# Optimization experiments

Measured on AMD Instinct MI355X. Metric: run time of the kernel, lower is better.

Reference implementation:

```python
import jax, jax.numpy as jnp
import numpy as np

DIM = 1024
HEADS = 16
HEAD_DIM = DIM // HEADS
EPS = 1e-5


def setup_inputs() -> dict:
    key = jax.random.key(0)
    ks = jax.random.split(key, 4)
    N, L = 4, 2048
    x = jax.random.normal(ks[0], (N, L, DIM), dtype=jnp.float32)
    # causal mask: True means masked (strictly upper triangle)
    attn_mask = jnp.triu(jnp.ones((L, L), dtype=jnp.bool_), k=1)[None, None, :, :]
    w_qkv = jax.random.normal(ks[1], (3 * DIM, DIM), dtype=jnp.float32) * (DIM ** -0.5)
    w_proj = jax.random.normal(ks[2], (DIM, DIM), dtype=jnp.float32) * (DIM ** -0.5)
    b_proj = jnp.zeros((DIM,), dtype=jnp.float32)
    q_gamma = jnp.ones((HEAD_DIM,), dtype=jnp.float32)
    q_beta = jnp.zeros((HEAD_DIM,), dtype=jnp.float32)
    k_gamma = jnp.ones((HEAD_DIM,), dtype=jnp.float32)
    k_beta = jnp.zeros((HEAD_DIM,), dtype=jnp.float32)
    return {"x": x, "attn_mask": attn_mask, "w_qkv": w_qkv, "w_proj": w_proj,
            "b_proj": b_proj, "q_gamma": q_gamma, "q_beta": q_beta,
            "k_gamma": k_gamma, "k_beta": k_beta}


def _layernorm(h, gamma, beta):
    mu = jnp.mean(h, axis=-1, keepdims=True)
    var = jnp.mean(jnp.square(h - mu), axis=-1, keepdims=True)
    return (h - mu) * jax.lax.rsqrt(var + EPS) * gamma + beta


def reference(x, attn_mask, w_qkv, w_proj, b_proj, q_gamma, q_beta, k_gamma, k_beta):
    N, L, D = x.shape
    H, hd = HEADS, HEAD_DIM
    scale = hd ** -0.5
    qkv = jnp.einsum('nld,ed->nle', x, w_qkv)  # [N, L, 3D]
    qkv = qkv.reshape(N, L, 3, H, hd).transpose(2, 0, 3, 1, 4)  # [3, N, H, L, hd]
    q, k, v = qkv[0], qkv[1], qkv[2]
    q = _layernorm(q, q_gamma, q_beta)
    k = _layernorm(k, k_gamma, k_beta)
    scores = jnp.einsum('nhqd,nhkd->nhqk', q * scale, k)
    scores = scores + jnp.where(attn_mask, -jnp.inf, 0.0).astype(scores.dtype)
    attn = jax.nn.softmax(scores, axis=-1)
    out = jnp.einsum('nhqk,nhkd->nhqd', attn, v)  # [N, H, L, hd]
    out = out.transpose(0, 2, 1, 3).reshape(N, L, D)
    return jnp.einsum('nld,ed->nle', out, w_proj) + b_proj
```

## Files before the change

kernel.cpp:

```cpp
#include <hip/hip_runtime.h>


using f16x8 = __attribute__((ext_vector_type(8))) _Float16;
using f16x4 = __attribute__((ext_vector_type(4))) _Float16;
using f16x2 = __attribute__((ext_vector_type(2))) _Float16;
using f32x4 = __attribute__((ext_vector_type(4))) float;
using f32x16 = __attribute__((ext_vector_type(16))) float;
using u32x4 = __attribute__((ext_vector_type(4))) unsigned int;

#define MFMA16(a, b, c) __builtin_amdgcn_mfma_f32_16x16x32_f16(a, b, c, 0, 0, 0)
#define MFMA32(a, b, c) __builtin_amdgcn_mfma_f32_32x32x16_f16(a, b, c, 0, 0, 0)

__device__ __forceinline__ void gload_lds16(const void* g, void* l) {
  __builtin_amdgcn_global_load_lds(
      (const __attribute__((address_space(1))) unsigned int*)g,
      (__attribute__((address_space(3))) unsigned int*)l, 16, 0, 0);
}

__device__ __forceinline__ float dot2acc(unsigned int pk, float c) {
#if __has_builtin(__builtin_amdgcn_fdot2)
  const f16x2 ones = {(_Float16)1.f, (_Float16)1.f};
  return __builtin_amdgcn_fdot2(__builtin_bit_cast(f16x2, pk), ones, c, false);
#else
  f16x2 v = __builtin_bit_cast(f16x2, pk);
  return c + (float)v[0] + (float)v[1];
#endif
}

__global__ __launch_bounds__(256) void convert_all_kernel(
    const float* __restrict__ x, const float* __restrict__ wq,
    const float* __restrict__ wp, _Float16* __restrict__ xb,
    _Float16* __restrict__ wqb, _Float16* __restrict__ wpb) {
  long i = ((long)blockIdx.x * 256 + threadIdx.x) * 8;
  const float* src;
  _Float16* dst;
  if (i < 8388608) {
    src = x; dst = xb;
  } else if (i < 8388608 + 3145728) {
    src = wq + (i - 8388608); dst = wqb + (i - 8388608); i = 0;
  } else {
    src = wp + (i - 11534336); dst = wpb + (i - 11534336); i = 0;
  }
  float4 a = *(const float4*)(src + i);
  float4 b = *(const float4*)(src + i + 4);
  f16x8 o;
  o[0] = (_Float16)a.x; o[1] = (_Float16)a.y; o[2] = (_Float16)a.z; o[3] = (_Float16)a.w;
  o[4] = (_Float16)b.x; o[5] = (_Float16)b.y; o[6] = (_Float16)b.z; o[7] = (_Float16)b.w;
  *(f16x8*)(dst + i) = o;
}

template <int MODE>
__global__ __launch_bounds__(256, 3) void gemm_bt(
    const _Float16* __restrict__ A, const _Float16* __restrict__ B,
    void* __restrict__ Cout, _Float16* __restrict__ Vt,
    const float* __restrict__ bias,
    const float* __restrict__ qg, const float* __restrict__ qb,
    const float* __restrict__ kg, const float* __restrict__ kb,
    int M, int N, int K) {
  __shared__ __align__(16) char smem[49152];
  const int tid = threadIdx.x;
  const int w = tid >> 6, lane = tid & 63;
  const int c = lane & 15, g = lane >> 4;
  const long mbase = (long)blockIdx.x * 128;
  const int by = (MODE == 1) ? (int)((blockIdx.y + 16) % 24) : (int)blockIdx.y;
  const long nbase = (long)by * 128;
  const int wm = (w >> 1) * 64, wn = (w & 1) * 64;
  const int sr4 = lane >> 2;
  const int scol = ((lane & 3) ^ ((lane >> 3) & 3)) * 8;
  const int sg = (g ^ ((c >> 1) & 3)) * 8;
  const char* pAr = smem + (wm + c) * 64 + sg * 2;
  const char* pBr = smem + 24576 + (wn + c) * 64 + sg * 2;

#define GSTAGE(off_, kt_)                                                     \
  {                                                                           \
    const int kk_ = (kt_) * 32;                                               \
    _Pragma("unroll") for (int i = 0; i < 2; ++i) {                           \
      const int arow = w * 32 + i * 16 + sr4;                                 \
      gload_lds16(A + (mbase + arow) * K + kk_ + scol,                        \
                  smem + (off_) + (w * 2 + i) * 1024);                        \
    }                                                                         \
    _Pragma("unroll") for (int j = 0; j < 2; ++j) {                           \
      const int brow = w * 32 + j * 16 + sr4;                                 \
      gload_lds16(B + (nbase + brow) * K + kk_ + scol,                        \
                  smem + 24576 + (off_) + (w * 2 + j) * 1024);                \
    }                                                                         \
  }

  f32x4 acc[4][4];
#pragma unroll
  for (int i = 0; i < 4; ++i)
#pragma unroll
    for (int j = 0; j < 4; ++j) acc[i][j] = f32x4{0.f, 0.f, 0.f, 0.f};

  const int nk = K >> 5;
  GSTAGE(0, 0);
  GSTAGE(8192, 1);
  int rOff = 0, sOff = 16384;
  for (int kt = 0; kt < nk; ++kt) {
    if (kt + 1 < nk) {
      asm volatile("s_waitcnt vmcnt(4)" ::: "memory");
    } else {
      asm volatile("s_waitcnt vmcnt(0)" ::: "memory");
    }
    __builtin_amdgcn_sched_barrier(0);
    __builtin_amdgcn_s_barrier();
    __builtin_amdgcn_sched_barrier(0);
    f16x8 af[4], bfr[4];
#pragma unroll
    for (int mt = 0; mt < 4; ++mt)
      af[mt] = *(const f16x8*)(pAr + rOff + mt * 1024);
#pragma unroll
    for (int nt = 0; nt < 4; ++nt)
      bfr[nt] = *(const f16x8*)(pBr + rOff + nt * 1024);
    if (kt + 2 < nk) GSTAGE(sOff, kt + 2);
#pragma unroll
    for (int mt = 0; mt < 4; ++mt)
#pragma unroll
      for (int nt = 0; nt < 4; ++nt)
        acc[mt][nt] = MFMA16(af[mt], bfr[nt], acc[mt][nt]);
    rOff = (rOff == 16384) ? 0 : rOff + 8192;
    sOff = (sOff == 16384) ? 0 : sOff + 8192;
  }
#undef GSTAGE

  if constexpr (MODE == 1) {
    const int region = by >> 3;
    if (region == 2) {
      __syncthreads();
      _Float16* T = (_Float16*)smem;
#pragma unroll
      for (int nt = 0; nt < 4; ++nt) {
        const int dloc = wn + nt * 16 + c;
#pragma unroll
        for (int mt = 0; mt < 4; ++mt) {
          const int lloc = wm + mt * 16 + g * 4;
          f16x4 o;
#pragma unroll
          for (int r = 0; r < 4; ++r) o[r] = (_Float16)acc[mt][nt][r];
          *(f16x4*)(T + dloc * 136 + lloc) = o;
        }
      }
      __syncthreads();
      const long n = mbase >> 11;
      const long lbase = mbase & 2047;
      const int chunk = tid & 15;
      const int rbase = tid >> 4;
#pragma unroll
      for (int i = 0; i < 8; ++i) {
        const int row = rbase + i * 16;
        const long dcol = (nbase - 2048) + row;
        *(f16x8*)(Vt + (n * 1024 + dcol) * 2048 + lbase + chunk * 8) =
            *(const f16x8*)(T + row * 136 + chunk * 8);
      }
      return;
    }
    const float* gamma = region ? kg : qg;
    const float* beta = region ? kb : qb;
    float gam[4], bet[4];
#pragma unroll
    for (int nt = 0; nt < 4; ++nt) {
      gam[nt] = gamma[nt * 16 + c];
      bet[nt] = beta[nt * 16 + c];
    }
    const float sc = region ? 1.f : 0.1803368801111204f;
#pragma unroll
    for (int mt = 0; mt < 4; ++mt)
#pragma unroll
      for (int r = 0; r < 4; ++r) {
        float s1 = 0.f, s2 = 0.f;
#pragma unroll
        for (int nt = 0; nt < 4; ++nt) {
          const float v = acc[mt][nt][r];
          s1 += v;
          s2 += v * v;
        }
#pragma unroll
        for (int msk = 1; msk < 16; msk <<= 1) {
          s1 += __shfl_xor(s1, msk);
          s2 += __shfl_xor(s2, msk);
        }
        const float mu = s1 * 0.015625f;
        const float rstd = rsqrtf(s2 * 0.015625f - mu * mu + 1e-5f);
#pragma unroll
        for (int nt = 0; nt < 4; ++nt)
          acc[mt][nt][r] =
              ((acc[mt][nt][r] - mu) * rstd * gam[nt] + bet[nt]) * sc;
      }
#pragma unroll
    for (int nt = 0; nt < 4; ++nt) {
      const long col = nbase + wn + nt * 16 + c;
#pragma unroll
      for (int mt = 0; mt < 4; ++mt)
#pragma unroll
        for (int r = 0; r < 4; ++r) {
          const long row = mbase + wm + mt * 16 + g * 4 + r;
          ((_Float16*)Cout)[row * N + col] = (_Float16)acc[mt][nt][r];
        }
    }
  } else {
#pragma unroll
    for (int nt = 0; nt < 4; ++nt) {
      const long col = nbase + wn + nt * 16 + c;
      const float bv = bias ? bias[col] : 0.f;
#pragma unroll
      for (int mt = 0; mt < 4; ++mt)
#pragma unroll
        for (int r = 0; r < 4; ++r) {
          const long row = mbase + wm + mt * 16 + g * 4 + r;
          ((float*)Cout)[row * N + col] = acc[mt][nt][r] + bv;
        }
    }
  }
}

__global__ __launch_bounds__(256, 3) void attn_kernel(
    const _Float16* __restrict__ qkv, const _Float16* __restrict__ Vt,
    _Float16* __restrict__ Ob) {
  __shared__ __align__(16) char lds[49152];
  const int w = threadIdx.x >> 6;
  const int lane = threadIdx.x & 63;
  const int c5 = lane & 31;
  const int hi = lane >> 5;
  const int lin = (int)(blockIdx.x + 64 * blockIdx.y);
  const int nh = (lin & 7) * 8 + ((lin >> 3) & 7);
  const long n = nh >> 4;
  const int h = nh & 15;
  const int qtile = 15 - (lin >> 6);
  const int qlo_blk = qtile * 128;
  const int qlo = qlo_blk + w * 32;
  const int qrow = qlo + c5;

  const _Float16* Qp = qkv + n * 2048 * 3072 + h * 64;
  const _Float16* Kq = Qp + 1024;
  const _Float16* Vp = Vt + (long)nh * 64 * 2048;

  const int sr8 = lane >> 3;
  const int scol = ((lane & 7) ^ sr8) * 8;

  const int nkv_blk = (qlo_blk + 191) >> 6;
  const int nkv_w = (qlo + 95) >> 6;

#define STAGE(OFF, kv_)                                                        \
  {                                                                            \
    const int kb_ = (kv_) * 64;                                                \
    _Pragma("unroll") for (int i = 0; i < 2; ++i) {                            \
      const int idx = w * 2 + i;                                               \
      const int row = idx * 8 + sr8;                                           \
      gload_lds16(Kq + (long)(kb_ + row) * 3072 + scol,                        \
                  lds + (OFF) + idx * 1024);                                   \
      gload_lds16(Vp + (long)row * 2048 + kb_ + scol,                          \
                  lds + (OFF) + 8192 + idx * 1024);                            \
    }                                                                          \
  }

  f16x8 qf[4];
#pragma unroll
  for (int dc = 0; dc < 4; ++dc)
    qf[dc] = *(const f16x8*)(Qp + (long)qrow * 3072 + dc * 16 + hi * 8);

  f32x16 negM;
#pragma unroll
  for (int r = 0; r < 16; ++r) negM[r] = -12.0f;

  f32x16 acc[2];
#pragma unroll
  for (int db = 0; db < 2; ++db)
#pragma unroll
    for (int r = 0; r < 16; ++r) acc[db][r] = 0.f;
  float ls = 0.f;

  const int swr = c5 & 7;
  const char* Lb[4];
#pragma unroll
  for (int j = 0; j < 4; ++j)
    Lb[j] = lds + c5 * 128 + (((j * 2 + hi) ^ swr) << 4);

#define COMPUTE(OFF, kv_)                                                      \
  {                                                                            \
    const int kbase = (kv_) * 64;                                              \
    f32x16 s0, s1;                                                             \
    __builtin_amdgcn_s_setprio(1);                                             \
    {                                                                          \
      f16x8 kf0 = *(const f16x8*)(Lb[0] + (OFF));                              \
      f16x8 kf1 = *(const f16x8*)(Lb[0] + (OFF) + 4096);                       \
      s0 = MFMA32(kf0, qf[0], negM);                                           \
      s1 = MFMA32(kf1, qf[0], negM);                                           \
    }                                                                          \
    _Pragma("unroll") for (int dc = 1; dc < 4; ++dc) {                         \
      f16x8 kf0 = *(const f16x8*)(Lb[dc] + (OFF));                             \
      f16x8 kf1 = *(const f16x8*)(Lb[dc] + (OFF) + 4096);                      \
      s0 = MFMA32(kf0, qf[dc], s0);                                            \
      s1 = MFMA32(kf1, qf[dc], s1);                                            \
    }                                                                          \
    __builtin_amdgcn_s_setprio(0);                                             \
    if (kbase + 63 > qlo) {                                                    \
      _Pragma("unroll") for (int r = 0; r < 16; ++r) {                         \
        const int mv = (r & 3) + 8 * (r >> 2) + 4 * hi;                        \
        if (kbase + mv > qrow) s0[r] = -1e30f;                                 \
        if (kbase + 32 + mv > qrow) s1[r] = -1e30f;                            \
      }                                                                        \
    }                                                                          \
    _Pragma("unroll") for (int r = 0; r < 16; ++r) {                           \
      s0[r] = exp2f(s0[r]);                                                    \
      s1[r] = exp2f(s1[r]);                                                    \
    }                                                                          \
    unsigned int pk0[4][2], pk1[4][2];                                         \
    _Pragma("unroll") for (int r2 = 0; r2 < 4; ++r2)                           \
        _Pragma("unroll") for (int p = 0; p < 2; ++p) {                        \
      pk0[r2][p] = __builtin_bit_cast(                                         \
          unsigned int, __builtin_amdgcn_cvt_pkrtz(s0[4 * r2 + 2 * p],         \
                                                   s0[4 * r2 + 2 * p + 1]));   \
      pk1[r2][p] = __builtin_bit_cast(                                         \
          unsigned int, __builtin_amdgcn_cvt_pkrtz(s1[4 * r2 + 2 * p],         \
                                                   s1[4 * r2 + 2 * p + 1]));   \
    }                                                                          \
    _Pragma("unroll") for (int r2 = 0; r2 < 4; ++r2)                           \
        _Pragma("unroll") for (int p = 0; p < 2; ++p) {                        \
      ls = dot2acc(pk0[r2][p], ls);                                            \
      ls = dot2acc(pk1[r2][p], ls);                                            \
    }                                                                          \
    f16x8 pB[4];                                                               \
    _Pragma("unroll") for (int kk = 0; kk < 4; ++kk) {                         \
      const int rx = (kk & 1) * 2;                                             \
      unsigned int x0 = (kk < 2) ? pk0[rx][0] : pk1[rx][0];                    \
      unsigned int y0 = (kk < 2) ? pk0[rx + 1][0] : pk1[rx + 1][0];            \
      unsigned int x1 = (kk < 2) ? pk0[rx][1] : pk1[rx][1];                    \
      unsigned int y1 = (kk < 2) ? pk0[rx + 1][1] : pk1[rx + 1][1];            \
      asm("v_permlane32_swap_b32 %0, %1" : "+v"(x0), "+v"(y0));                \
      asm("v_permlane32_swap_b32 %0, %1" : "+v"(x1), "+v"(y1));                \
      pB[kk] = __builtin_bit_cast(f16x8, u32x4{x0, x1, y0, y1});               \
    }                                                                          \
    __builtin_amdgcn_s_setprio(1);                                             \
    _Pragma("unroll") for (int db = 0; db < 2; ++db)                           \
        _Pragma("unroll") for (int kk = 0; kk < 4; ++kk) {                     \
      f16x8 vf = *(const f16x8*)(Lb[kk] + (OFF) + 8192 + db * 4096);           \
      acc[db] = MFMA32(vf, pB[kk], acc[db]);                                   \
    }                                                                          \
    __builtin_amdgcn_s_setprio(0);                                             \
  }

  STAGE(0, 0);
  STAGE(16384, 1);
  int rOff = 0, sOff = 32768;
  for (int kv = 0; kv < nkv_blk; ++kv) {
    if (kv + 1 < nkv_blk) {
      asm volatile("s_waitcnt vmcnt(4)" ::: "memory");
    } else {
      asm volatile("s_waitcnt vmcnt(0)" ::: "memory");
    }
    __builtin_amdgcn_sched_barrier(0);
    __builtin_amdgcn_s_barrier();
    __builtin_amdgcn_sched_barrier(0);
    if (kv + 2 < nkv_blk) STAGE(sOff, kv + 2);
    if (kv < nkv_w) COMPUTE(rOff, kv);
    rOff = (rOff == 32768) ? 0 : rOff + 16384;
    sOff = (sOff == 32768) ? 0 : sOff + 16384;
  }
#undef COMPUTE
#undef STAGE

  const float lsr = ls + __shfl_xor(ls, 32);
  const float inv = 1.f / lsr;
  _Float16* ob = Ob + ((long)(n * 2048) + qrow) * 1024 + h * 64 + 4 * hi;
#pragma unroll
  for (int db = 0; db < 2; ++db)
#pragma unroll
    for (int r2 = 0; r2 < 4; ++r2) {
      f16x4 o;
#pragma unroll
      for (int j = 0; j < 4; ++j)
        o[j] = (_Float16)(acc[db][4 * r2 + j] * inv);
      *(f16x4*)(ob + db * 32 + 8 * r2) = o;
    }
}

extern "C" void kernel_launch(void* const* d_in, const int* in_sizes, int n_in,
                              void* d_out, int out_size, void* d_ws, size_t ws_size,
                              hipStream_t stream) {
  const float* x = (const float*)d_in[0];
  const float* w_qkv = (const float*)d_in[2];
  const float* w_proj = (const float*)d_in[3];
  const float* b_proj = (const float*)d_in[4];
  const float* qg = (const float*)d_in[5];
  const float* qb = (const float*)d_in[6];
  const float* kg = (const float*)d_in[7];
  const float* kb = (const float*)d_in[8];

  char* ws = (char*)d_ws;
  _Float16* xb     = (_Float16*)(ws + 0);
  _Float16* wqkvb  = (_Float16*)(ws + 16777216);
  _Float16* wprojb = (_Float16*)(ws + 23068672);
  _Float16* qkvh   = (_Float16*)(ws + 25165824);
  _Float16* Vt     = (_Float16*)(ws + 75497472);
  _Float16* Ob     = xb;

  convert_all_kernel<<<6144, 256, 0, stream>>>(x, w_qkv, w_proj,
                                               xb, wqkvb, wprojb);

  gemm_bt<1><<<dim3(64, 24), 256, 0, stream>>>(xb, wqkvb, qkvh, Vt, nullptr,
                                               qg, qb, kg, kb, 8192, 3072, 1024);
  attn_kernel<<<dim3(64, 16), 256, 0, stream>>>(qkvh, Vt, Ob);
  gemm_bt<0><<<dim3(64, 8), 256, 0, stream>>>(Ob, wprojb, d_out, nullptr, b_proj,
                                              nullptr, nullptr, nullptr, nullptr,
                                              8192, 1024, 1024);
}
```

Measured before the change: 186.3 us.

## Give each wave its own LDS pipeline and 32-key tiles, removing block barriers

Each wave now stages its own K/V tiles into a private 16KB LDS region with double buffering over 32-key tiles. Block-wide barriers go away and each wave iterates only up to its own causal limit, instead of sharing 64-key tiles across the block. The costs are that the four waves load K/V redundantly instead of sharing, LDS rises to 64KB, and the launch bound drops to 2 blocks per CU. MFMA work per tile is halved, so loop overhead and wait points double.

```diff
diff --git a/kernel.cpp b/kernel.cpp
--- a/kernel.cpp
+++ b/kernel.cpp
@@ -213,10 +213,10 @@
   }
 }
 
-__global__ __launch_bounds__(256, 3) void attn_kernel(
+__global__ __launch_bounds__(256, 2) void attn_kernel(
     const _Float16* __restrict__ qkv, const _Float16* __restrict__ Vt,
     _Float16* __restrict__ Ob) {
-  __shared__ __align__(16) char lds[49152];
+  __shared__ __align__(16) char lds[65536];
   const int w = threadIdx.x >> 6;
   const int lane = threadIdx.x & 63;
   const int c5 = lane & 31;
@@ -226,30 +226,31 @@
   const long n = nh >> 4;
   const int h = nh & 15;
   const int qtile = 15 - (lin >> 6);
-  const int qlo_blk = qtile * 128;
-  const int qlo = qlo_blk + w * 32;
+  const int unit = qtile * 4 + w;
+  const int qlo = unit * 32;
   const int qrow = qlo + c5;
 
   const _Float16* Qp = qkv + n * 2048 * 3072 + h * 64;
   const _Float16* Kq = Qp + 1024;
   const _Float16* Vp = Vt + (long)nh * 64 * 2048;
 
+  char* myLds = lds + w * 16384;
   const int sr8 = lane >> 3;
   const int scol = ((lane & 7) ^ sr8) * 8;
-
-  const int nkv_blk = (qlo_blk + 191) >> 6;
-  const int nkv_w = (qlo + 95) >> 6;
-
-#define STAGE(OFF, kv_)                                                        \
+  const int vscol = ((lane & 3) ^ ((lane >> 3) & 3)) * 8;
+
+  const int nkv = unit + 1;
+
+#define STAGE(BOFF, t_)                                                        \
   {                                                                            \
-    const int kb_ = (kv_) * 64;                                                \
-    _Pragma("unroll") for (int i = 0; i < 2; ++i) {                            \
-      const int idx = w * 2 + i;                                               \
-      const int row = idx * 8 + sr8;                                           \
-      gload_lds16(Kq + (long)(kb_ + row) * 3072 + scol,                        \
-                  lds + (OFF) + idx * 1024);                                   \
-      gload_lds16(Vp + (long)row * 2048 + kb_ + scol,                          \
-                  lds + (OFF) + 8192 + idx * 1024);                            \
+    const int kb_ = (t_) * 32;                                                 \
+    _Pragma("unroll") for (int i = 0; i < 4; ++i) {                            \
+      const int krow = i * 8 + sr8;                                            \
+      gload_lds16(Kq + (long)(kb_ + krow) * 3072 + scol,                       \
+                  myLds + (BOFF) + i * 1024);                                  \
+      const int vrow = i * 16 + (lane >> 2);                                   \
+      gload_lds16(Vp + (long)vrow * 2048 + kb_ + vscol,                        \
+                  myLds + (BOFF) + 4096 + i * 1024);                           \
     }                                                                          \
   }
 
@@ -270,91 +271,83 @@
   float ls = 0.f;
 
   const int swr = c5 & 7;
-  const char* Lb[4];
+  const int vxor = (c5 >> 1) & 3;
+  const char* Lk[4];
 #pragma unroll
   for (int j = 0; j < 4; ++j)
-    Lb[j] = lds + c5 * 128 + (((j * 2 + hi) ^ swr) << 4);
-
-#define COMPUTE(OFF, kv_)                                                      \
+    Lk[j] = myLds + c5 * 128 + (((j * 2 + hi) ^ swr) << 4);
+  const char* Lv[4];
+#pragma unroll
+  for (int db = 0; db < 2; ++db)
+#pragma unroll
+    for (int kk = 0; kk < 2; ++kk)
+      Lv[db * 2 + kk] = myLds + 4096 + (db * 32 + c5) * 64 +
+                        (((kk * 2 + hi) ^ vxor) << 4);
+
+#define COMPUTE(BOFF, t_)                                                      \
   {                                                                            \
-    const int kbase = (kv_) * 64;                                              \
-    f32x16 s0, s1;                                                             \
+    const int kbase = (t_) * 32;                                               \
+    f32x16 s0;                                                                 \
     __builtin_amdgcn_s_setprio(1);                                             \
     {                                                                          \
-      f16x8 kf0 = *(const f16x8*)(Lb[0] + (OFF));                              \
-      f16x8 kf1 = *(const f16x8*)(Lb[0] + (OFF) + 4096);                       \
-      s0 = MFMA32(kf0, qf[0], negM);                                           \
-      s1 = MFMA32(kf1, qf[0], negM);                                           \
+      f16x8 kf = *(const f16x8*)(Lk[0] + (BOFF));                              \
+      s0 = MFMA32(kf, qf[0], negM);                                            \
     }                                                                          \
     _Pragma("unroll") for (int dc = 1; dc < 4; ++dc) {                         \
-      f16x8 kf0 = *(const f16x8*)(Lb[dc] + (OFF));                             \
-      f16x8 kf1 = *(const f16x8*)(Lb[dc] + (OFF) + 4096);                      \
-      s0 = MFMA32(kf0, qf[dc], s0);                                            \
-      s1 = MFMA32(kf1, qf[dc], s1);                                            \
+      f16x8 kf = *(const f16x8*)(Lk[dc] + (BOFF));                             \
+      s0 = MFMA32(kf, qf[dc], s0);                                             \
     }                                                                          \
     __builtin_amdgcn_s_setprio(0);                                             \
-    if (kbase + 63 > qlo) {                                                    \
+    if (kbase + 31 > qlo) {                                                    \
       _Pragma("unroll") for (int r = 0; r < 16; ++r) {                         \
         const int mv = (r & 3) + 8 * (r >> 2) + 4 * hi;                        \
         if (kbase + mv > qrow) s0[r] = -1e30f;                                 \
-        if (kbase + 32 + mv > qrow) s1[r] = -1e30f;                            \
       }                                                                        \
     }                                                                          \
-    _Pragma("unroll") for (int r = 0; r < 16; ++r) {                           \
-      s0[r] = exp2f(s0[r]);                                                    \
-      s1[r] = exp2f(s1[r]);                                                    \
-    }                                                                          \
-    unsigned int pk0[4][2], pk1[4][2];                                         \
+    _Pragma("unroll") for (int r = 0; r < 16; ++r) s0[r] = exp2f(s0[r]);       \
+    unsigned int pk0[4][2];                                                    \
     _Pragma("unroll") for (int r2 = 0; r2 < 4; ++r2)                           \
         _Pragma("unroll") for (int p = 0; p < 2; ++p) {                        \
       pk0[r2][p] = __builtin_bit_cast(                                         \
           unsigned int, __builtin_amdgcn_cvt_pkrtz(s0[4 * r2 + 2 * p],         \
                                                    s0[4 * r2 + 2 * p + 1]));   \
-      pk1[r2][p] = __builtin_bit_cast(                                         \
-          unsigned int, __builtin_amdgcn_cvt_pkrtz(s1[4 * r2 + 2 * p],         \
-                                                   s1[4 * r2 + 2 * p + 1]));   \
-    }                                                                          \
-    _Pragma("unroll") for (int r2 = 0; r2 < 4; ++r2)                           \
-        _Pragma("unroll") for (int p = 0; p < 2; ++p) {                        \
       ls = dot2acc(pk0[r2][p], ls);                                            \
-      ls = dot2acc(pk1[r2][p], ls);                                            \
-    }                                                                          \
-    f16x8 pB[4];                                                               \
-    _Pragma("unroll") for (int kk = 0; kk < 4; ++kk) {                         \
-      const int rx = (kk & 1) * 2;                                             \
-      unsigned int x0 = (kk < 2) ? pk0[rx][0] : pk1[rx][0];                    \
-      unsigned int y0 = (kk < 2) ? pk0[rx + 1][0] : pk1[rx + 1][0];            \
-      unsigned int x1 = (kk < 2) ? pk0[rx][1] : pk1[rx][1];                    \
-      unsigned int y1 = (kk < 2) ? pk0[rx + 1][1] : pk1[rx + 1][1];            \
+    }                                                                          \
+    f16x8 pB[2];                                                               \
+    _Pragma("unroll") for (int kk = 0; kk < 2; ++kk) {                         \
+      const int rx = kk * 2;                                                   \
+      unsigned int x0 = pk0[rx][0];                                            \
+      unsigned int y0 = pk0[rx + 1][0];                                        \
+      unsigned int x1 = pk0[rx][1];                                            \
+      unsigned int y1 = pk0[rx + 1][1];                                        \
       asm("v_permlane32_swap_b32 %0, %1" : "+v"(x0), "+v"(y0));                \
       asm("v_permlane32_swap_b32 %0, %1" : "+v"(x1), "+v"(y1));                \
       pB[kk] = __builtin_bit_cast(f16x8, u32x4{x0, x1, y0, y1});               \
     }                                                                          \
     __builtin_amdgcn_s_setprio(1);                                             \
     _Pragma("unroll") for (int db = 0; db < 2; ++db)                           \
-        _Pragma("unroll") for (int kk = 0; kk < 4; ++kk) {                     \
-      f16x8 vf = *(const f16x8*)(Lb[kk] + (OFF) + 8192 + db * 4096);           \
+        _Pragma("unroll") for (int kk = 0; kk < 2; ++kk) {                     \
+      f16x8 vf = *(const f16x8*)(Lv[db * 2 + kk] + (BOFF));                    \
       acc[db] = MFMA32(vf, pB[kk], acc[db]);                                   \
     }                                                                          \
     __builtin_amdgcn_s_setprio(0);                                             \
   }
 
   STAGE(0, 0);
-  STAGE(16384, 1);
-  int rOff = 0, sOff = 32768;
-  for (int kv = 0; kv < nkv_blk; ++kv) {
-    if (kv + 1 < nkv_blk) {
-      asm volatile("s_waitcnt vmcnt(4)" ::: "memory");
+  if (nkv > 1) STAGE(8192, 1);
+  for (int t = 0; t < nkv; ++t) {
+    if (t + 1 < nkv) {
+      asm volatile("s_waitcnt vmcnt(8)" ::: "memory");
     } else {
       asm volatile("s_waitcnt vmcnt(0)" ::: "memory");
     }
     __builtin_amdgcn_sched_barrier(0);
-    __builtin_amdgcn_s_barrier();
-    __builtin_amdgcn_sched_barrier(0);
-    if (kv + 2 < nkv_blk) STAGE(sOff, kv + 2);
-    if (kv < nkv_w) COMPUTE(rOff, kv);
-    rOff = (rOff == 32768) ? 0 : rOff + 16384;
-    sOff = (sOff == 32768) ? 0 : sOff + 16384;
+    COMPUTE((t & 1) * 8192, t);
+    if (t + 2 < nkv) {
+      asm volatile("s_waitcnt lgkmcnt(0)" ::: "memory");
+      __builtin_amdgcn_sched_barrier(0);
+      STAGE((t & 1) * 8192, t + 2);
+    }
   }
 #undef COMPUTE
 #undef STAGE
```

Measured after the change: 203.4 us. 9.2% more time.

## Rewrite QKV GEMM with 256x256 tiles, 512 threads and phased LDS pipeline

Applied to the files above, without the earlier changes.

Replaces the templated 128x128 GEMM for the QKV projection with a dedicated kernel that uses 256x256 output tiles, 8 waves and 128 KB of LDS double-buffering over 64-wide K steps. The loads for the next K step are split into four phases, interleaved with MFMA work, and gated by explicit vmcnt waits, barriers and s_setprio. The aim is more data reuse per loaded byte and better overlap of global-to-LDS copies with matrix math. The cost is a grid of only 384 blocks, which may hurt occupancy and wave balance. The V-transpose epilogue is reworked to run in two passes, and the output projection becomes a separate non-templated kernel.

```diff
diff --git a/kernel.cpp b/kernel.cpp
--- a/kernel.cpp
+++ b/kernel.cpp
@@ -49,21 +49,205 @@
   *(f16x8*)(dst + i) = o;
 }
 
-template <int MODE>
-__global__ __launch_bounds__(256, 3) void gemm_bt(
+__global__ __launch_bounds__(512, 2) void gemm_qkv(
     const _Float16* __restrict__ A, const _Float16* __restrict__ B,
-    void* __restrict__ Cout, _Float16* __restrict__ Vt,
-    const float* __restrict__ bias,
+    _Float16* __restrict__ qkvh, _Float16* __restrict__ Vt,
     const float* __restrict__ qg, const float* __restrict__ qb,
-    const float* __restrict__ kg, const float* __restrict__ kb,
+    const float* __restrict__ kg, const float* __restrict__ kb) {
+  __shared__ __align__(16) char smem[131072];
+  const int tid = threadIdx.x;
+  const int w = tid >> 6, lane = tid & 63;
+  const int c = lane & 15, g = lane >> 4;
+  const int wr = w >> 2, wc = w & 3;
+  const long mbase = (long)blockIdx.x * 256;
+  const int by = (int)((blockIdx.y + 8) % 12);
+  const long nbase = (long)by * 256;
+  const int srow = tid >> 3;
+  const int scol = ((tid & 7) ^ ((tid >> 3) & 7)) * 8;
+  const int swr8 = c & 7;
+  const char* LA[2];
+  const char* LB[2];
+#pragma unroll
+  for (int ks = 0; ks < 2; ++ks) {
+    LA[ks] = smem + wr * 16384 + c * 128 + (((ks * 4 + g) ^ swr8) << 4);
+    LB[ks] = smem + 65536 + (wc >> 1) * 16384 + ((wc & 1) * 64 + c) * 128 +
+             (((ks * 4 + g) ^ swr8) << 4);
+  }
+
+#define ST_A(DD, HH, RR, KT)                                                  \
+  gload_lds16(                                                                \
+      A + (mbase + (HH) * 128 + (RR) * 64 + srow) * 1024 + (KT) * 64 + scol,  \
+      smem + (DD) + (HH) * 16384 + (RR) * 8192 + w * 1024)
+#define ST_B(DD, HH, RR, KT)                                                  \
+  gload_lds16(                                                                \
+      B + (nbase + (HH) * 128 + (RR) * 64 + srow) * 1024 + (KT) * 64 + scol,  \
+      smem + 65536 + (DD) + (HH) * 16384 + (RR) * 8192 + w * 1024)
+
+  f32x4 acc[8][4];
+#pragma unroll
+  for (int i = 0; i < 8; ++i)
+#pragma unroll
+    for (int j = 0; j < 4; ++j) acc[i][j] = f32x4{0.f, 0.f, 0.f, 0.f};
+
+#define PHASE(P)                                                              \
+  {                                                                           \
+    f16x8 bf0[4], bf1[4], af00, af01, af10, af11;                             \
+    _Pragma("unroll") for (int nt = 0; nt < 4; ++nt) {                        \
+      bf0[nt] = *(const f16x8*)(LB[0] + rd + nt * 2048);                      \
+      bf1[nt] = *(const f16x8*)(LB[1] + rd + nt * 2048);                      \
+    }                                                                         \
+    af00 = *(const f16x8*)(LA[0] + rd + (2 * (P)) * 2048);                    \
+    af01 = *(const f16x8*)(LA[1] + rd + (2 * (P)) * 2048);                    \
+    af10 = *(const f16x8*)(LA[0] + rd + (2 * (P) + 1) * 2048);                \
+    af11 = *(const f16x8*)(LA[1] + rd + (2 * (P) + 1) * 2048);                \
+    __builtin_amdgcn_s_setprio(1);                                            \
+    _Pragma("unroll") for (int nt = 0; nt < 4; ++nt) {                        \
+      acc[2 * (P)][nt] = MFMA16(af00, bf0[nt], acc[2 * (P)][nt]);             \
+      acc[2 * (P)][nt] = MFMA16(af01, bf1[nt], acc[2 * (P)][nt]);             \
+      acc[2 * (P) + 1][nt] = MFMA16(af10, bf0[nt], acc[2 * (P) + 1][nt]);     \
+      acc[2 * (P) + 1][nt] = MFMA16(af11, bf1[nt], acc[2 * (P) + 1][nt]);     \
+    }                                                                         \
+    __builtin_amdgcn_s_setprio(0);                                            \
+  }
+
+#define BARRIER()                      \
+  __builtin_amdgcn_sched_barrier(0);   \
+  __builtin_amdgcn_s_barrier();        \
+  __builtin_amdgcn_sched_barrier(0)
+
+  const int nk = 16;
+  ST_B(0, 0, 0, 0); ST_B(0, 0, 1, 0); ST_B(0, 1, 0, 0); ST_B(0, 1, 1, 0);
+  ST_A(0, 0, 0, 0); ST_A(0, 1, 0, 0); ST_A(0, 0, 1, 0); ST_A(0, 1, 1, 0);
+  int rd = 0, sd = 32768;
+  for (int kt = 0; kt < nk; ++kt) {
+    const bool more = (kt + 1 < nk);
+    asm volatile("s_waitcnt vmcnt(2)" ::: "memory");
+    BARRIER();
+    if (more) { ST_B(sd, 0, 0, kt + 1); ST_B(sd, 0, 1, kt + 1); }
+    PHASE(0);
+    if (more) {
+      asm volatile("s_waitcnt vmcnt(4)" ::: "memory");
+    } else {
+      asm volatile("s_waitcnt vmcnt(2)" ::: "memory");
+    }
+    BARRIER();
+    if (more) { ST_B(sd, 1, 0, kt + 1); ST_B(sd, 1, 1, kt + 1); }
+    PHASE(1);
+    if (more) {
+      asm volatile("s_waitcnt vmcnt(4)" ::: "memory");
+    } else {
+      asm volatile("s_waitcnt vmcnt(0)" ::: "memory");
+    }
+    BARRIER();
+    if (more) { ST_A(sd, 0, 0, kt + 1); ST_A(sd, 1, 0, kt + 1); }
+    PHASE(2);
+    if (more) {
+      asm volatile("s_waitcnt vmcnt(6)" ::: "memory");
+    } else {
+      asm volatile("s_waitcnt vmcnt(0)" ::: "memory");
+    }
+    BARRIER();
+    if (more) { ST_A(sd, 0, 1, kt + 1); ST_A(sd, 1, 1, kt + 1); }
+    PHASE(3);
+    rd ^= 32768;
+    sd ^= 32768;
+  }
+#undef PHASE
+#undef BARRIER
+#undef ST_A
+#undef ST_B
+
+  const int region = by >> 2;
+  if (region == 2) {
+    __syncthreads();
+    _Float16* T = (_Float16*)smem;
+    const long n = mbase >> 11;
+    const long lbase = mbase & 2047;
+    const int chunk = tid & 31;
+    const int rbase = tid >> 5;
+#pragma unroll
+    for (int p2 = 0; p2 < 2; ++p2) {
+      if ((wc >> 1) == p2) {
+#pragma unroll
+        for (int nt = 0; nt < 4; ++nt) {
+          const int dloc = (wc & 1) * 64 + nt * 16 + c;
+#pragma unroll
+          for (int mt = 0; mt < 8; ++mt) {
+            const int lloc = wr * 128 + mt * 16 + g * 4;
+            f16x4 o;
+#pragma unroll
+            for (int r = 0; r < 4; ++r) o[r] = (_Float16)acc[mt][nt][r];
+            *(f16x4*)(T + dloc * 264 + lloc) = o;
+          }
+        }
+      }
+      __syncthreads();
+#pragma unroll
+      for (int i = 0; i < 8; ++i) {
+        const int row = rbase + i * 16;
+        const long dcol = (nbase - 2048) + p2 * 128 + row;
+        *(f16x8*)(Vt + (n * 1024 + dcol) * 2048 + lbase + chunk * 8) =
+            *(const f16x8*)(T + row * 264 + chunk * 8);
+      }
+      __syncthreads();
+    }
+    return;
+  }
+  const float* gamma = region ? kg : qg;
+  const float* beta = region ? kb : qb;
+  float gam[4], bet[4];
+#pragma unroll
+  for (int nt = 0; nt < 4; ++nt) {
+    gam[nt] = gamma[nt * 16 + c];
+    bet[nt] = beta[nt * 16 + c];
+  }
+  const float sc = region ? 1.f : 0.1803368801111204f;
+#pragma unroll
+  for (int mt = 0; mt < 8; ++mt)
+#pragma unroll
+    for (int r = 0; r < 4; ++r) {
+      float s1 = 0.f, s2 = 0.f;
+#pragma unroll
+      for (int nt = 0; nt < 4; ++nt) {
+        const float v = acc[mt][nt][r];
+        s1 += v;
+        s2 += v * v;
+      }
+#pragma unroll
+      for (int msk = 1; msk < 16; msk <<= 1) {
+        s1 += __shfl_xor(s1, msk);
+        s2 += __shfl_xor(s2, msk);
+      }
+      const float mu = s1 * 0.015625f;
+      const float rstd = rsqrtf(s2 * 0.015625f - mu * mu + 1e-5f);
+#pragma unroll
+      for (int nt = 0; nt < 4; ++nt)
+        acc[mt][nt][r] =
+            ((acc[mt][nt][r] - mu) * rstd * gam[nt] + bet[nt]) * sc;
+    }
+#pragma unroll
+  for (int nt = 0; nt < 4; ++nt) {
+    const long col = nbase + wc * 64 + nt * 16 + c;
+#pragma unroll
+    for (int mt = 0; mt < 8; ++mt)
+#pragma unroll
+      for (int r = 0; r < 4; ++r) {
+        const long row = mbase + wr * 128 + mt * 16 + g * 4 + r;
+        qkvh[row * 3072 + col] = (_Float16)acc[mt][nt][r];
+      }
+  }
+}
+
+__global__ __launch_bounds__(256, 3) void gemm_proj(
+    const _Float16* __restrict__ A, const _Float16* __restrict__ B,
+    float* __restrict__ Cout, const float* __restrict__ bias,
     int M, int N, int K) {
   __shared__ __align__(16) char smem[49152];
   const int tid = threadIdx.x;
   const int w = tid >> 6, lane = tid & 63;
   const int c = lane & 15, g = lane >> 4;
   const long mbase = (long)blockIdx.x * 128;
-  const int by = (MODE == 1) ? (int)((blockIdx.y + 16) % 24) : (int)blockIdx.y;
-  const long nbase = (long)by * 128;
+  const long nbase = (long)blockIdx.y * 128;
   const int wm = (w >> 1) * 64, wn = (w & 1) * 64;
   const int sr4 = lane >> 2;
   const int scol = ((lane & 3) ^ ((lane >> 3) & 3)) * 8;
@@ -123,93 +307,17 @@
   }
 #undef GSTAGE
 
-  if constexpr (MODE == 1) {
-    const int region = by >> 3;
-    if (region == 2) {
-      __syncthreads();
-      _Float16* T = (_Float16*)smem;
-#pragma unroll
-      for (int nt = 0; nt < 4; ++nt) {
-        const int dloc = wn + nt * 16 + c;
-#pragma unroll
-        for (int mt = 0; mt < 4; ++mt) {
-          const int lloc = wm + mt * 16 + g * 4;
-          f16x4 o;
-#pragma unroll
-          for (int r = 0; r < 4; ++r) o[r] = (_Float16)acc[mt][nt][r];
-          *(f16x4*)(T + dloc * 136 + lloc) = o;
-        }
+#pragma unroll
+  for (int nt = 0; nt < 4; ++nt) {
+    const long col = nbase + wn + nt * 16 + c;
+    const float bv = bias ? bias[col] : 0.f;
+#pragma unroll
+    for (int mt = 0; mt < 4; ++mt)
+#pragma unroll
+      for (int r = 0; r < 4; ++r) {
+        const long row = mbase + wm + mt * 16 + g * 4 + r;
+        Cout[row * N + col] = acc[mt][nt][r] + bv;
       }
-      __syncthreads();
-      const long n = mbase >> 11;
-      const long lbase = mbase & 2047;
-      const int chunk = tid & 15;
-      const int rbase = tid >> 4;
-#pragma unroll
-      for (int i = 0; i < 8; ++i) {
-        const int row = rbase + i * 16;
-        const long dcol = (nbase - 2048) + row;
-        *(f16x8*)(Vt + (n * 1024 + dcol) * 2048 + lbase + chunk * 8) =
-            *(const f16x8*)(T + row * 136 + chunk * 8);
-      }
-      return;
-    }
-    const float* gamma = region ? kg : qg;
-    const float* beta = region ? kb : qb;
-    float gam[4], bet[4];
-#pragma unroll
-    for (int nt = 0; nt < 4; ++nt) {
-      gam[nt] = gamma[nt * 16 + c];
-      bet[nt] = beta[nt * 16 + c];
-    }
-    const float sc = region ? 1.f : 0.1803368801111204f;
-#pragma unroll
-    for (int mt = 0; mt < 4; ++mt)
-#pragma unroll
-      for (int r = 0; r < 4; ++r) {
-        float s1 = 0.f, s2 = 0.f;
-#pragma unroll
-        for (int nt = 0; nt < 4; ++nt) {
-          const float v = acc[mt][nt][r];
-          s1 += v;
-          s2 += v * v;
-        }
-#pragma unroll
-        for (int msk = 1; msk < 16; msk <<= 1) {
-          s1 += __shfl_xor(s1, msk);
-          s2 += __shfl_xor(s2, msk);
-        }
-        const float mu = s1 * 0.015625f;
-        const float rstd = rsqrtf(s2 * 0.015625f - mu * mu + 1e-5f);
-#pragma unroll
-        for (int nt = 0; nt < 4; ++nt)
-          acc[mt][nt][r] =
-              ((acc[mt][nt][r] - mu) * rstd * gam[nt] + bet[nt]) * sc;
-      }
-#pragma unroll
-    for (int nt = 0; nt < 4; ++nt) {
-      const long col = nbase + wn + nt * 16 + c;
-#pragma unroll
-      for (int mt = 0; mt < 4; ++mt)
-#pragma unroll
-        for (int r = 0; r < 4; ++r) {
-          const long row = mbase + wm + mt * 16 + g * 4 + r;
-          ((_Float16*)Cout)[row * N + col] = (_Float16)acc[mt][nt][r];
-        }
-    }
-  } else {
-#pragma unroll
-    for (int nt = 0; nt < 4; ++nt) {
-      const long col = nbase + wn + nt * 16 + c;
-      const float bv = bias ? bias[col] : 0.f;
-#pragma unroll
-      for (int mt = 0; mt < 4; ++mt)
-#pragma unroll
-        for (int r = 0; r < 4; ++r) {
-          const long row = mbase + wm + mt * 16 + g * 4 + r;
-          ((float*)Cout)[row * N + col] = acc[mt][nt][r] + bv;
-        }
-    }
   }
 }
 
@@ -397,10 +505,9 @@
   convert_all_kernel<<<6144, 256, 0, stream>>>(x, w_qkv, w_proj,
                                                xb, wqkvb, wprojb);
 
-  gemm_bt<1><<<dim3(64, 24), 256, 0, stream>>>(xb, wqkvb, qkvh, Vt, nullptr,
-                                               qg, qb, kg, kb, 8192, 3072, 1024);
+  gemm_qkv<<<dim3(32, 12), 512, 0, stream>>>(xb, wqkvb, qkvh, Vt,
+                                             qg, qb, kg, kb);
   attn_kernel<<<dim3(64, 16), 256, 0, stream>>>(qkvh, Vt, Ob);
-  gemm_bt<0><<<dim3(64, 8), 256, 0, stream>>>(Ob, wprojb, d_out, nullptr, b_proj,
-                                              nullptr, nullptr, nullptr, nullptr,
-                                              8192, 1024, 1024);
-}
+  gemm_proj<<<dim3(64, 8), 256, 0, stream>>>(Ob, wprojb, (float*)d_out, b_proj,
+                                             8192, 1024, 1024);
+}
```

Result: slower. 190.6 us (+2.3%).
